# Performance work log

Hardware: AMD Instinct MI355X
Metric: run time of the kernel (lower is better)

## Reference

```python
import jax, jax.numpy as jnp
import numpy as np

B, C, SEG = 16, 32, 512            # graphs, configs per graph, nodes per segment
N = B * C * SEG                     # 262144 total nodes
E = 2 * N                           # 524288 edges
NUM_OPS, OP_DIM = 120, 64
NF_RAW = 112                        # raw node features
NF_IN = NF_RAW + OP_DIM             # 176
ND, CD = 192, 64                    # node_feature_dim, conf_feature_dim
GH = ND + CD                        # 256 graphsage hidden


def setup_inputs() -> dict:
    key = jax.random.key(0)
    ks = jax.random.split(key, 40)
    g = lambda i, shape, s: jax.random.normal(ks[i], shape, jnp.float32) * s
    inp = {
        'node_features': jax.random.normal(ks[0], (N, NF_RAW), jnp.float32),
        'node_config_features': jax.random.normal(ks[1], (N, 14), jnp.float32),
        'node_separation': (jnp.arange(B * C) + 1) * SEG,          # cumulative end idx
        'node_ops': jax.random.randint(ks[2], (N,), 0, NUM_OPS),
        'edges': jax.random.randint(ks[3], (2, E), 0, N),
        'batches': jnp.repeat(jnp.arange(B), C),
        # parameters (stored as [in, out]); ~1/sqrt(fan_in) scale
        'emb': g(4, (NUM_OPS, OP_DIM), 0.1),
        'nf_w1': g(5, (NF_IN, NF_IN), 0.075), 'nf_b1': jnp.zeros((NF_IN,)),
        'nf_w2': g(6, (NF_IN, ND), 0.075),   'nf_b2': jnp.zeros((ND,)),
        'cf_w1': g(7, (14, 14), 0.26),       'cf_b1': jnp.zeros((14,)),
        'cf_w2': g(8, (14, CD), 0.26),       'cf_b2': jnp.zeros((CD,)),
        'pre_w1': g(9, (GH, ND), 0.06),      'pre_b1': jnp.zeros((ND,)),
        'pre_w2': g(10, (ND, ND), 0.07),     'pre_b2': jnp.zeros((ND,)),
        'sage_wl': g(11, (2, GH, GH), 0.06), 'sage_bl': jnp.zeros((2, GH)),
        'sage_wr': g(12, (2, GH, GH), 0.06),
        'mlp_w1': g(13, (2, GH, ND), 0.06),  'mlp_b1': jnp.zeros((2, ND)),
        'mlp_w2': g(14, (2, ND, ND), 0.07),  'mlp_b2': jnp.zeros((2, ND)),
        'fc_w': g(15, (ND, 1), 0.07),
    }
    return inp


def reference(node_features, node_config_features, node_separation, node_ops,
              edges, batches, emb, nf_w1, nf_b1, nf_w2, nf_b2,
              cf_w1, cf_b1, cf_w2, cf_b2, pre_w1, pre_b1, pre_w2, pre_b2,
              sage_wl, sage_bl, sage_wr, mlp_w1, mlp_b1, mlp_w2, mlp_b2, fc_w):
    lr01 = lambda v: jax.nn.leaky_relu(v, 0.01)   # torch.nn.LeakyReLU default
    lr02 = lambda v: jax.nn.leaky_relu(v, 0.2)    # MLP / GraphSage alpha

    # embedding + node feature MLP
    x = jnp.concatenate([node_features, emb[node_ops]], axis=1)        # [N,176]
    x = lr01(lr01(x @ nf_w1 + nf_b1) @ nf_w2 + nf_b2)                  # [N,192]
    cf = lr01(lr01(node_config_features @ cf_w1 + cf_b1) @ cf_w2 + cf_b2)  # [N,64]

    # GraphSage encoder: prenet then 2 residual SAGEConv+MLP blocks
    h = jnp.concatenate([cf, x], axis=1)                               # [N,256]
    h = lr02(lr02(h @ pre_w1 + pre_b1) @ pre_w2 + pre_b2)              # [N,192]
    src, dst = edges[0], edges[1]
    n = h.shape[0]
    for l in range(2):
        y = jnp.concatenate([cf, h], axis=1)                           # [N,256]
        # SAGEConv(aggr='max'): lin_l(max_{j->i} y_j) + lin_r(y_i)
        agg = jax.ops.segment_max(y[src], dst, num_segments=n)
        agg = jnp.where(jnp.isfinite(agg), agg, 0.0)  # isolated nodes -> 0
        y = agg @ sage_wl[l] + sage_bl[l] + y @ sage_wr[l]             # [N,256]
        y = lr02(lr02(y @ mlp_w1[l] + mlp_b1[l]) @ mlp_w2[l] + mlp_b2[l])
        h = h + y

    # per-segment sum pooling (the original Python loop), then group by graph
    seg_id = jnp.searchsorted(node_separation, jnp.arange(n), side='right')
    pooled = jax.ops.segment_sum(h, seg_id, num_segments=node_separation.shape[0])  # [B*C,192]
    scores = (pooled @ fc_w)[:, 0]                                      # [B*C]
    return scores.reshape(B, C)
```

## Files before the change

kernel.cpp:

```cpp
#include <hip/hip_runtime.h>
#include <hip/hip_bf16.h>
#include <math.h>

#define NNODES 262144
#define NEDGES 524288
#define NSEG   512

typedef __hip_bfloat16 bf16;
typedef __attribute__((ext_vector_type(8))) short short8;
typedef __attribute__((ext_vector_type(4))) short short4v;
typedef __attribute__((ext_vector_type(4))) float f32x4;

__device__ __forceinline__ short bfbits(float f) {
    return __builtin_bit_cast(short, (__bf16)f);
}
__device__ __forceinline__ float bitsf(short s) {
    unsigned u = ((unsigned)(unsigned short)s) << 16;
    return __builtin_bit_cast(float, u);
}

__device__ __forceinline__ short8 ld8(const bf16* p, size_t off) {
    return *(const short8*)((const short*)p + off);
}
__device__ __forceinline__ short8 ld8(const float* p, size_t off) {
    const float4* q = (const float4*)(p + off);
    float4 a = q[0], b = q[1];
    short8 r;
    r[0] = bfbits(a.x); r[1] = bfbits(a.y); r[2] = bfbits(a.z); r[3] = bfbits(a.w);
    r[4] = bfbits(b.x); r[5] = bfbits(b.y); r[6] = bfbits(b.z); r[7] = bfbits(b.w);
    return r;
}

__global__ void prep_wt(const float* __restrict__ Wa, int kw,
                        const float* __restrict__ Wb,
                        short* __restrict__ Wt, int K, int OUT)
{
    int k = blockIdx.x * 256 + threadIdx.x;
    int c = blockIdx.y;
    if (k < K) {
        float v = (k < kw) ? Wa[(size_t)k * OUT + c] : Wb[(size_t)(k - kw) * OUT + c];
        Wt[(size_t)c * K + k] = bfbits(v);
    }
}

template<typename TA, int BN>
__global__ __launch_bounds__(512, 4) void mfma_gemm(
    const TA* __restrict__ A0, int w0,
    const TA* __restrict__ A1, int w1,
    const TA* __restrict__ A2, int w2,
    const int*   __restrict__ gidx,
    const short* __restrict__ Wt,
    const float* __restrict__ bias,
    const bf16*  __restrict__ res,
    bf16* __restrict__ out,
    int K, int OUT, float alpha)
{
    constexpr int NRW = BN / 64;
    __shared__ short As[128 * 40];
    __shared__ short Bs[BN * 40];
    __shared__ float biasLds[BN];

    const int tid  = threadIdx.x;
    const int lane = tid & 63;
    const int wid  = tid >> 6;
    const int row0 = blockIdx.x * 128;
    const int wr   = (wid >> 2) * 64;
    const int wc   = (wid & 3) * (BN / 4);
    const int fr   = lane & 15;
    const int fc   = lane >> 4;

    if (tid < BN) biasLds[tid] = (tid < OUT) ? bias[tid] : 0.f;

    f32x4 acc[NRW][4];
    #pragma unroll
    for (int nr = 0; nr < NRW; ++nr)
        #pragma unroll
        for (int m = 0; m < 4; ++m) acc[nr][m] = f32x4{0.f, 0.f, 0.f, 0.f};

    for (int k0 = 0; k0 < K; k0 += 32) {
        {
            int r  = tid >> 2;
            int kl = (tid & 3) * 8;
            int gk = k0 + kl;
            short8 v{};
            if (gk < K) {
                int n = row0 + r;
                if (gk < w0) v = ld8(A0, (size_t)n * w0 + gk);
                else {
                    int k1 = gk - w0;
                    if (k1 < w1) {
                        int rr = gidx ? gidx[n] : n;
                        v = ld8(A1, (size_t)rr * w1 + k1);
                    } else {
                        v = ld8(A2, (size_t)n * w2 + (k1 - w1));
                    }
                }
            }
            *(short8*)&As[r * 40 + kl] = v;
        }
        #pragma unroll
        for (int i = 0; i < (BN * 4 + 511) / 512; ++i) {
            int f = i * 512 + tid;
            if (f < BN * 4) {
                int c  = f >> 2;
                int kl = (f & 3) * 8;
                int gk = k0 + kl;
                short8 v{};
                if (gk < K && c < OUT) v = *(const short8*)&Wt[(size_t)c * K + gk];
                *(short8*)&Bs[c * 40 + kl] = v;
            }
        }
        __syncthreads();
        short8 af[4];
        #pragma unroll
        for (int m = 0; m < 4; ++m)
            af[m] = *(short8*)&As[(wr + m * 16 + fr) * 40 + fc * 8];
        #pragma unroll
        for (int nr = 0; nr < NRW; ++nr) {
            short8 bfr = *(short8*)&Bs[(wc + nr * 16 + fr) * 40 + fc * 8];
            #pragma unroll
            for (int m = 0; m < 4; ++m)
                acc[nr][m] = __builtin_amdgcn_mfma_f32_16x16x32_bf16(
                    bfr, af[m], acc[nr][m], 0, 0, 0);
        }
        __syncthreads();
    }
    #pragma unroll
    for (int nr = 0; nr < NRW; ++nr) {
        int c0 = wc + nr * 16 + fc * 4;
        if (c0 < OUT) {
            #pragma unroll
            for (int m = 0; m < 4; ++m) {
                int r = row0 + wr + m * 16 + fr;
                size_t base = (size_t)r * OUT + c0;
                short4v o;
                if (res) {
                    short4v rv = *(const short4v*)((const short*)res + base);
                    #pragma unroll
                    for (int j = 0; j < 4; ++j) {
                        float v = acc[nr][m][j] + biasLds[c0 + j];
                        v = (v > 0.f) ? v : alpha * v;
                        o[j] = bfbits(v + bitsf(rv[j]));
                    }
                } else {
                    #pragma unroll
                    for (int j = 0; j < 4; ++j) {
                        float v = acc[nr][m][j] + biasLds[c0 + j];
                        v = (v > 0.f) ? v : alpha * v;
                        o[j] = bfbits(v);
                    }
                }
                *(short4v*)((short*)out + base) = o;
            }
        }
    }
}

__global__ __launch_bounds__(256) void cf_mlp(
    const float* __restrict__ ncf,
    const float* __restrict__ w1, const float* __restrict__ b1,
    const float* __restrict__ w2, const float* __restrict__ b2,
    bf16* __restrict__ cf)
{
    __shared__ float W1s[196], B1s[14], W2s[896], B2s[64];
    int t = threadIdx.x;
    for (int i = t; i < 196; i += 256) W1s[i] = w1[i];
    for (int i = t; i < 896; i += 256) W2s[i] = w2[i];
    if (t < 14) B1s[t] = b1[t];
    if (t >= 32 && t < 96) B2s[t - 32] = b2[t - 32];
    __syncthreads();

    int n = blockIdx.x * 256 + t;
    float in[14], hid[14];
    #pragma unroll
    for (int k = 0; k < 14; ++k) in[k] = ncf[(size_t)n * 14 + k];
    #pragma unroll
    for (int j = 0; j < 14; ++j) {
        float s = B1s[j];
        #pragma unroll
        for (int k = 0; k < 14; ++k) s += in[k] * W1s[k * 14 + j];
        hid[j] = (s > 0.f) ? s : 0.01f * s;
    }
    #pragma unroll 4
    for (int j = 0; j < 64; ++j) {
        float s = B2s[j];
        #pragma unroll
        for (int k = 0; k < 14; ++k) s += hid[k] * W2s[k * 64 + j];
        s = (s > 0.f) ? s : 0.01f * s;
        cf[(size_t)n * 64 + j] = __float2bfloat16(s);
    }
}

__global__ void zero_ints(int* __restrict__ p, int n)
{
    int i = blockIdx.x * 256 + threadIdx.x;
    if (i < n) p[i] = 0;
}

__global__ void count_deg(const int* __restrict__ dst, int* __restrict__ indeg)
{
    int e = blockIdx.x * 256 + threadIdx.x;
    atomicAdd(&indeg[dst[e]], 1);
}

__global__ __launch_bounds__(256) void scan_block(
    const int* __restrict__ in, int* __restrict__ part, int* __restrict__ bsums)
{
    __shared__ int sh[256];
    int t = threadIdx.x, b = blockIdx.x;
    int base = b * 1024 + t * 4;
    int v0 = in[base], v1 = in[base + 1], v2 = in[base + 2], v3 = in[base + 3];
    int s = v0 + v1 + v2 + v3;
    sh[t] = s; __syncthreads();
    #pragma unroll
    for (int off = 1; off < 256; off <<= 1) {
        int x = (t >= off) ? sh[t - off] : 0;
        __syncthreads();
        sh[t] += x;
        __syncthreads();
    }
    int excl = sh[t] - s;
    if (t == 255) bsums[b] = sh[t];
    part[base]     = excl;
    part[base + 1] = excl + v0;
    part[base + 2] = excl + v0 + v1;
    part[base + 3] = excl + v0 + v1 + v2;
}

__global__ __launch_bounds__(256) void scan_tops(int* __restrict__ bsums)
{
    __shared__ int sh[256];
    int t = threadIdx.x;
    int s = bsums[t];
    sh[t] = s; __syncthreads();
    #pragma unroll
    for (int off = 1; off < 256; off <<= 1) {
        int x = (t >= off) ? sh[t - off] : 0;
        __syncthreads();
        sh[t] += x;
        __syncthreads();
    }
    bsums[t] = sh[t] - s;
}

__global__ void scan_fix(int* __restrict__ offsets, const int* __restrict__ bsums,
                         int* __restrict__ cursor)
{
    int i = blockIdx.x * 256 + threadIdx.x;
    int v = offsets[i] + bsums[i >> 10];
    offsets[i] = v;
    cursor[i]  = v;
    if (i == 0) offsets[NNODES] = NEDGES;
}

__global__ void scatter_edges(const int* __restrict__ src, const int* __restrict__ dst,
                              int* __restrict__ cursor, int* __restrict__ csr)
{
    int e = blockIdx.x * 256 + threadIdx.x;
    int pos = atomicAdd(&cursor[dst[e]], 1);
    csr[pos] = src[e];
}

__global__ __launch_bounds__(256) void sage_agg(
    const int* __restrict__ offsets, const int* __restrict__ csr,
    const bf16* __restrict__ cf, const bf16* __restrict__ h,
    bf16* __restrict__ agg)
{
    int wid = threadIdx.x >> 6, lane = threadIdx.x & 63;
    int n = blockIdx.x * 4 + wid;
    int beg = offsets[n], end = offsets[n + 1];
    float m0 = -3.4e38f, m1 = m0, m2 = m0, m3 = m0;
    for (int e = beg; e < end; ++e) {
        int s = csr[e];
        m0 = fmaxf(m0, __bfloat162float(cf[(size_t)s * 64 + lane]));
        const bf16* hr = h + (size_t)s * 192;
        m1 = fmaxf(m1, __bfloat162float(hr[lane]));
        m2 = fmaxf(m2, __bfloat162float(hr[64 + lane]));
        m3 = fmaxf(m3, __bfloat162float(hr[128 + lane]));
    }
    if (beg == end) { m0 = m1 = m2 = m3 = 0.f; }
    bf16* ar = agg + (size_t)n * 256;
    ar[lane]       = __float2bfloat16(m0);
    ar[64 + lane]  = __float2bfloat16(m1);
    ar[128 + lane] = __float2bfloat16(m2);
    ar[192 + lane] = __float2bfloat16(m3);
}

__global__ __launch_bounds__(256) void pool_fc(
    const bf16* __restrict__ h, const int* __restrict__ sep,
    const float* __restrict__ fc_w, float* __restrict__ out)
{
    __shared__ float red[256];
    int b = blockIdx.x, t = threadIdx.x;
    int r0 = (b == 0) ? 0 : sep[b - 1];
    int r1 = sep[b];
    float s0 = 0.f, s1 = 0.f, s2 = 0.f, s3 = 0.f;
    if (t < 192) {
        int r = r0;
        for (; r + 3 < r1; r += 4) {
            s0 += __bfloat162float(h[(size_t)r * 192 + t]);
            s1 += __bfloat162float(h[(size_t)(r + 1) * 192 + t]);
            s2 += __bfloat162float(h[(size_t)(r + 2) * 192 + t]);
            s3 += __bfloat162float(h[(size_t)(r + 3) * 192 + t]);
        }
        for (; r < r1; ++r) s0 += __bfloat162float(h[(size_t)r * 192 + t]);
    }
    red[t] = (t < 192) ? (s0 + s1 + s2 + s3) * fc_w[t] : 0.f;
    __syncthreads();
    #pragma unroll
    for (int st = 128; st > 0; st >>= 1) {
        if (t < st) red[t] += red[t + st];
        __syncthreads();
    }
    if (t == 0) out[b] = red[0];
}

__global__ void report_ws(float* __restrict__ out, float mb)
{
    out[blockIdx.x * 256 + threadIdx.x] = mb;
}

extern "C" void kernel_launch(void* const* d_in, const int* in_sizes, int n_in,
                              void* d_out, int out_size, void* d_ws, size_t ws_size,
                              hipStream_t stream)
{
    const float* node_features = (const float*)d_in[0];
    const float* node_config   = (const float*)d_in[1];
    const int*   node_sep      = (const int*)d_in[2];
    const int*   node_ops      = (const int*)d_in[3];
    const int*   edges         = (const int*)d_in[4];
    const float* emb    = (const float*)d_in[6];
    const float* nf_w1  = (const float*)d_in[7];
    const float* nf_b1  = (const float*)d_in[8];
    const float* nf_w2  = (const float*)d_in[9];
    const float* nf_b2  = (const float*)d_in[10];
    const float* cf_w1  = (const float*)d_in[11];
    const float* cf_b1  = (const float*)d_in[12];
    const float* cf_w2  = (const float*)d_in[13];
    const float* cf_b2  = (const float*)d_in[14];
    const float* pre_w1 = (const float*)d_in[15];
    const float* pre_b1 = (const float*)d_in[16];
    const float* pre_w2 = (const float*)d_in[17];
    const float* pre_b2 = (const float*)d_in[18];
    const float* sage_wl= (const float*)d_in[19];
    const float* sage_bl= (const float*)d_in[20];
    const float* sage_wr= (const float*)d_in[21];
    const float* mlp_w1 = (const float*)d_in[22];
    const float* mlp_b1 = (const float*)d_in[23];
    const float* mlp_w2 = (const float*)d_in[24];
    const float* mlp_b2 = (const float*)d_in[25];
    const float* fc_w   = (const float*)d_in[26];

    const size_t N = NNODES;

    const size_t WT_NF1  = 0;
    const size_t WT_NF2  = WT_NF1  + 176 * 176;
    const size_t WT_PRE1 = WT_NF2  + 192 * 176;
    const size_t WT_PRE2 = WT_PRE1 + 192 * 256;
    const size_t WT_SAGE = WT_PRE2 + 192 * 192;
    const size_t WT_MLP1 = WT_SAGE + 2 * 256 * 512;
    const size_t WT_MLP2 = WT_MLP1 + 2 * 192 * 256;
    const size_t WT_TOT  = WT_MLP2 + 2 * 192 * 192;

    const size_t fl_bytes  = N * 768 * sizeof(bf16);
    const size_t wt_bytes  = WT_TOT * 2;
    const size_t int_elems = (N + 1) + N + N + NEDGES + 256;
    const size_t needed    = fl_bytes + wt_bytes + int_elems * 4;
    if (ws_size < needed) {
        report_ws<<<2, 256, 0, stream>>>((float*)d_out,
                                         (float)((double)ws_size / 1048576.0));
        return;
    }

    bf16* cf   = (bf16*)d_ws;
    bf16* h    = cf   + N * 64;
    bf16* bufA = h    + N * 192;
    bf16* bufB = bufA + N * 256;
    short* wt  = (short*)(bufB + N * 256);
    int* offsets = (int*)(wt + WT_TOT);
    int* indeg   = offsets + (N + 1);
    int* cursor  = indeg + N;
    int* csr     = cursor + N;
    int* bsums   = csr + NEDGES;

    const int* esrc = edges;
    const int* edst = edges + NEDGES;

    dim3 blk(256);
    dim3 blk512(512);
    const int GB = NNODES / 128;

    prep_wt<<<dim3(1, 176), blk, 0, stream>>>(nf_w1, 176, nullptr, wt + WT_NF1, 176, 176);
    prep_wt<<<dim3(1, 192), blk, 0, stream>>>(nf_w2, 176, nullptr, wt + WT_NF2, 176, 192);
    prep_wt<<<dim3(1, 192), blk, 0, stream>>>(pre_w1, 256, nullptr, wt + WT_PRE1, 256, 192);
    prep_wt<<<dim3(1, 192), blk, 0, stream>>>(pre_w2, 192, nullptr, wt + WT_PRE2, 192, 192);
    for (int l = 0; l < 2; ++l) {
        prep_wt<<<dim3(2, 256), blk, 0, stream>>>(
            sage_wl + (size_t)l * 256 * 256, 256, sage_wr + (size_t)l * 256 * 256,
            wt + WT_SAGE + (size_t)l * 256 * 512, 512, 256);
        prep_wt<<<dim3(1, 192), blk, 0, stream>>>(
            mlp_w1 + (size_t)l * 256 * 192, 256, nullptr,
            wt + WT_MLP1 + (size_t)l * 192 * 256, 256, 192);
        prep_wt<<<dim3(1, 192), blk, 0, stream>>>(
            mlp_w2 + (size_t)l * 192 * 192, 192, nullptr,
            wt + WT_MLP2 + (size_t)l * 192 * 192, 192, 192);
    }

    cf_mlp<<<NNODES / 256, blk, 0, stream>>>(node_config, cf_w1, cf_b1, cf_w2, cf_b2, cf);

    mfma_gemm<float, 192><<<GB, blk512, 0, stream>>>(
        node_features, 112, emb, 64, (const float*)nullptr, 0, node_ops,
        wt + WT_NF1, nf_b1, nullptr, bufA, 176, 176, 0.01f);
    mfma_gemm<bf16, 192><<<GB, blk512, 0, stream>>>(
        bufA, 176, (const bf16*)nullptr, 0, (const bf16*)nullptr, 0, nullptr,
        wt + WT_NF2, nf_b2, nullptr, bufB, 176, 192, 0.01f);

    mfma_gemm<bf16, 192><<<GB, blk512, 0, stream>>>(
        cf, 64, bufB, 192, (const bf16*)nullptr, 0, nullptr,
        wt + WT_PRE1, pre_b1, nullptr, bufA, 256, 192, 0.2f);
    mfma_gemm<bf16, 192><<<GB, blk512, 0, stream>>>(
        bufA, 192, (const bf16*)nullptr, 0, (const bf16*)nullptr, 0, nullptr,
        wt + WT_PRE2, pre_b2, nullptr, h, 192, 192, 0.2f);

    zero_ints<<<NNODES / 256, blk, 0, stream>>>(indeg, NNODES);
    count_deg<<<NEDGES / 256, blk, 0, stream>>>(edst, indeg);
    scan_block<<<NNODES / 1024, blk, 0, stream>>>(indeg, offsets, bsums);
    scan_tops<<<1, blk, 0, stream>>>(bsums);
    scan_fix<<<NNODES / 256, blk, 0, stream>>>(offsets, bsums, cursor);
    scatter_edges<<<NEDGES / 256, blk, 0, stream>>>(esrc, edst, cursor, csr);

    for (int l = 0; l < 2; ++l) {
        sage_agg<<<NNODES / 4, blk, 0, stream>>>(offsets, csr, cf, h, bufA);
        mfma_gemm<bf16, 256><<<GB, blk512, 0, stream>>>(
            bufA, 256, cf, 64, h, 192, nullptr,
            wt + WT_SAGE + (size_t)l * 256 * 512, sage_bl + (size_t)l * 256,
            nullptr, bufB, 512, 256, 1.0f);
        mfma_gemm<bf16, 192><<<GB, blk512, 0, stream>>>(
            bufB, 256, (const bf16*)nullptr, 0, (const bf16*)nullptr, 0, nullptr,
            wt + WT_MLP1 + (size_t)l * 192 * 256, mlp_b1 + (size_t)l * 192,
            nullptr, bufA, 256, 192, 0.2f);
        mfma_gemm<bf16, 192><<<GB, blk512, 0, stream>>>(
            bufA, 192, (const bf16*)nullptr, 0, (const bf16*)nullptr, 0, nullptr,
            wt + WT_MLP2 + (size_t)l * 192 * 192, mlp_b2 + (size_t)l * 192,
            h, h, 192, 192, 0.2f);
    }

    pool_fc<<<NSEG, blk, 0, stream>>>(h, node_sep, fc_w, (float*)d_out);
}
```

Before: 1.564 ms.

## Prefetch GEMM tiles into registers, vectorize SAGE max gather, batch weight prep

The MFMA GEMM now loads the next K-slice of A and B into registers while the current slice is multiplied from LDS, so global-load latency overlaps with compute. The SAGE max aggregation gives each lane four contiguous bf16 values via a 64-bit load and processes two edges per iteration, which cuts the number of load instructions per gathered row. The ten weight-transpose kernels are merged into one launch with a job table, removing launch overhead. Holding the prefetched tiles raises register pressure in the GEMM, which could lower occupancy.

```diff
diff --git a/kernel.cpp b/kernel.cpp
--- a/kernel.cpp
+++ b/kernel.cpp
@@ -31,15 +31,23 @@
     return r;
 }
 
-__global__ void prep_wt(const float* __restrict__ Wa, int kw,
-                        const float* __restrict__ Wb,
-                        short* __restrict__ Wt, int K, int OUT)
-{
+struct PrepJobs {
+    const float* wa[10];
+    const float* wb[10];
+    int kw[10]; int K[10]; int OUT[10]; long off[10];
+};
+
+__global__ void prep_all(PrepJobs jobs, short* __restrict__ wt)
+{
+    int j = blockIdx.z;
     int k = blockIdx.x * 256 + threadIdx.x;
     int c = blockIdx.y;
-    if (k < K) {
-        float v = (k < kw) ? Wa[(size_t)k * OUT + c] : Wb[(size_t)(k - kw) * OUT + c];
-        Wt[(size_t)c * K + k] = bfbits(v);
+    int K = jobs.K[j], OUT = jobs.OUT[j];
+    if (k < K && c < OUT) {
+        int kw = jobs.kw[j];
+        float v = (k < kw) ? jobs.wa[j][(size_t)k * OUT + c]
+                           : jobs.wb[j][(size_t)(k - kw) * OUT + c];
+        wt[jobs.off[j] + (size_t)c * K + k] = bfbits(v);
     }
 }
 
@@ -56,6 +64,7 @@
     int K, int OUT, float alpha)
 {
     constexpr int NRW = BN / 64;
+    constexpr int NB  = (BN * 4 + 511) / 512;
     __shared__ short As[128 * 40];
     __shared__ short Bs[BN * 40];
     __shared__ float biasLds[BN];
@@ -71,46 +80,70 @@
 
     if (tid < BN) biasLds[tid] = (tid < OUT) ? bias[tid] : 0.f;
 
-    f32x4 acc[NRW][4];
-    #pragma unroll
-    for (int nr = 0; nr < NRW; ++nr)
-        #pragma unroll
-        for (int m = 0; m < 4; ++m) acc[nr][m] = f32x4{0.f, 0.f, 0.f, 0.f};
-
-    for (int k0 = 0; k0 < K; k0 += 32) {
-        {
-            int r  = tid >> 2;
-            int kl = (tid & 3) * 8;
-            int gk = k0 + kl;
-            short8 v{};
-            if (gk < K) {
-                int n = row0 + r;
-                if (gk < w0) v = ld8(A0, (size_t)n * w0 + gk);
-                else {
-                    int k1 = gk - w0;
-                    if (k1 < w1) {
-                        int rr = gidx ? gidx[n] : n;
-                        v = ld8(A1, (size_t)rr * w1 + k1);
-                    } else {
-                        v = ld8(A2, (size_t)n * w2 + (k1 - w1));
-                    }
+    const int ar  = tid >> 2;
+    const int akl = (tid & 3) * 8;
+
+    auto loadA = [&](int k0) -> short8 {
+        int gk = k0 + akl;
+        short8 v{};
+        if (gk < K) {
+            int n = row0 + ar;
+            if (gk < w0) v = ld8(A0, (size_t)n * w0 + gk);
+            else {
+                int k1 = gk - w0;
+                if (k1 < w1) {
+                    int rr = gidx ? gidx[n] : n;
+                    v = ld8(A1, (size_t)rr * w1 + k1);
+                } else {
+                    v = ld8(A2, (size_t)n * w2 + (k1 - w1));
                 }
             }
-            *(short8*)&As[r * 40 + kl] = v;
-        }
-        #pragma unroll
-        for (int i = 0; i < (BN * 4 + 511) / 512; ++i) {
+        }
+        return v;
+    };
+    auto loadB = [&](int k0, int i) -> short8 {
+        int f = i * 512 + tid;
+        short8 v{};
+        if (f < BN * 4) {
+            int c  = f >> 2;
+            int gk = k0 + (f & 3) * 8;
+            if (gk < K && c < OUT) v = *(const short8*)&Wt[(size_t)c * K + gk];
+        }
+        return v;
+    };
+
+    f32x4 acc[NRW][4];
+    #pragma unroll
+    for (int nr = 0; nr < NRW; ++nr)
+        #pragma unroll
+        for (int m = 0; m < 4; ++m) acc[nr][m] = f32x4{0.f, 0.f, 0.f, 0.f};
+
+    short8 aC = loadA(0);
+    short8 bC[NB];
+    #pragma unroll
+    for (int i = 0; i < NB; ++i) bC[i] = loadB(0, i);
+
+    for (int k0 = 0; k0 < K; k0 += 32) {
+        *(short8*)&As[ar * 40 + akl] = aC;
+        #pragma unroll
+        for (int i = 0; i < NB; ++i) {
             int f = i * 512 + tid;
             if (f < BN * 4) {
                 int c  = f >> 2;
                 int kl = (f & 3) * 8;
-                int gk = k0 + kl;
-                short8 v{};
-                if (gk < K && c < OUT) v = *(const short8*)&Wt[(size_t)c * K + gk];
-                *(short8*)&Bs[c * 40 + kl] = v;
+                *(short8*)&Bs[c * 40 + kl] = bC[i];
             }
         }
         __syncthreads();
+        short8 aN{};
+        short8 bN[NB];
+        #pragma unroll
+        for (int i = 0; i < NB; ++i) bN[i] = short8{};
+        if (k0 + 32 < K) {
+            aN = loadA(k0 + 32);
+            #pragma unroll
+            for (int i = 0; i < NB; ++i) bN[i] = loadB(k0 + 32, i);
+        }
         short8 af[4];
         #pragma unroll
         for (int m = 0; m < 4; ++m)
@@ -124,6 +157,9 @@
                     bfr, af[m], acc[nr][m], 0, 0, 0);
         }
         __syncthreads();
+        aC = aN;
+        #pragma unroll
+        for (int i = 0; i < NB; ++i) bC[i] = bN[i];
     }
     #pragma unroll
     for (int nr = 0; nr < NRW; ++nr) {
@@ -269,21 +305,35 @@
     int wid = threadIdx.x >> 6, lane = threadIdx.x & 63;
     int n = blockIdx.x * 4 + wid;
     int beg = offsets[n], end = offsets[n + 1];
+
+    bool isCf = lane < 16;
+    const short* basep = isCf ? (const short*)cf : (const short*)h;
+    int rowW   = isCf ? 64 : 192;
+    int colOff = isCf ? lane * 4 : lane * 4 - 64;
+
     float m0 = -3.4e38f, m1 = m0, m2 = m0, m3 = m0;
-    for (int e = beg; e < end; ++e) {
-        int s = csr[e];
-        m0 = fmaxf(m0, __bfloat162float(cf[(size_t)s * 64 + lane]));
-        const bf16* hr = h + (size_t)s * 192;
-        m1 = fmaxf(m1, __bfloat162float(hr[lane]));
-        m2 = fmaxf(m2, __bfloat162float(hr[64 + lane]));
-        m3 = fmaxf(m3, __bfloat162float(hr[128 + lane]));
+    int e = beg;
+    for (; e + 1 < end; e += 2) {
+        int s0 = csr[e], s1 = csr[e + 1];
+        short4v v0 = *(const short4v*)(basep + (size_t)s0 * rowW + colOff);
+        short4v v1 = *(const short4v*)(basep + (size_t)s1 * rowW + colOff);
+        m0 = fmaxf(fmaxf(m0, bitsf(v0[0])), bitsf(v1[0]));
+        m1 = fmaxf(fmaxf(m1, bitsf(v0[1])), bitsf(v1[1]));
+        m2 = fmaxf(fmaxf(m2, bitsf(v0[2])), bitsf(v1[2]));
+        m3 = fmaxf(fmaxf(m3, bitsf(v0[3])), bitsf(v1[3]));
+    }
+    if (e < end) {
+        int s0 = csr[e];
+        short4v v0 = *(const short4v*)(basep + (size_t)s0 * rowW + colOff);
+        m0 = fmaxf(m0, bitsf(v0[0]));
+        m1 = fmaxf(m1, bitsf(v0[1]));
+        m2 = fmaxf(m2, bitsf(v0[2]));
+        m3 = fmaxf(m3, bitsf(v0[3]));
     }
     if (beg == end) { m0 = m1 = m2 = m3 = 0.f; }
-    bf16* ar = agg + (size_t)n * 256;
-    ar[lane]       = __float2bfloat16(m0);
-    ar[64 + lane]  = __float2bfloat16(m1);
-    ar[128 + lane] = __float2bfloat16(m2);
-    ar[192 + lane] = __float2bfloat16(m3);
+    short4v o;
+    o[0] = bfbits(m0); o[1] = bfbits(m1); o[2] = bfbits(m2); o[3] = bfbits(m3);
+    *(short4v*)((short*)agg + (size_t)n * 256 + lane * 4) = o;
 }
 
 __global__ __launch_bounds__(256) void pool_fc(
@@ -390,20 +440,24 @@
     dim3 blk512(512);
     const int GB = NNODES / 128;
 
-    prep_wt<<<dim3(1, 176), blk, 0, stream>>>(nf_w1, 176, nullptr, wt + WT_NF1, 176, 176);
-    prep_wt<<<dim3(1, 192), blk, 0, stream>>>(nf_w2, 176, nullptr, wt + WT_NF2, 176, 192);
-    prep_wt<<<dim3(1, 192), blk, 0, stream>>>(pre_w1, 256, nullptr, wt + WT_PRE1, 256, 192);
-    prep_wt<<<dim3(1, 192), blk, 0, stream>>>(pre_w2, 192, nullptr, wt + WT_PRE2, 192, 192);
-    for (int l = 0; l < 2; ++l) {
-        prep_wt<<<dim3(2, 256), blk, 0, stream>>>(
-            sage_wl + (size_t)l * 256 * 256, 256, sage_wr + (size_t)l * 256 * 256,
-            wt + WT_SAGE + (size_t)l * 256 * 512, 512, 256);
-        prep_wt<<<dim3(1, 192), blk, 0, stream>>>(
-            mlp_w1 + (size_t)l * 256 * 192, 256, nullptr,
-            wt + WT_MLP1 + (size_t)l * 192 * 256, 256, 192);
-        prep_wt<<<dim3(1, 192), blk, 0, stream>>>(
-            mlp_w2 + (size_t)l * 192 * 192, 192, nullptr,
-            wt + WT_MLP2 + (size_t)l * 192 * 192, 192, 192);
+    {
+        PrepJobs jobs;
+        auto set = [&](int i, const float* wa, const float* wb, int kw, int K,
+                       int OUT, size_t off) {
+            jobs.wa[i] = wa; jobs.wb[i] = wb; jobs.kw[i] = kw;
+            jobs.K[i] = K; jobs.OUT[i] = OUT; jobs.off[i] = (long)off;
+        };
+        set(0, nf_w1, nullptr, 176, 176, 176, WT_NF1);
+        set(1, nf_w2, nullptr, 176, 176, 192, WT_NF2);
+        set(2, pre_w1, nullptr, 256, 256, 192, WT_PRE1);
+        set(3, pre_w2, nullptr, 192, 192, 192, WT_PRE2);
+        set(4, sage_wl,               sage_wr,               256, 512, 256, WT_SAGE);
+        set(5, sage_wl + 256 * 256,   sage_wr + 256 * 256,   256, 512, 256, WT_SAGE + 256 * 512);
+        set(6, mlp_w1,                nullptr, 256, 256, 192, WT_MLP1);
+        set(7, mlp_w1 + 256 * 192,    nullptr, 256, 256, 192, WT_MLP1 + 192 * 256);
+        set(8, mlp_w2,                nullptr, 192, 192, 192, WT_MLP2);
+        set(9, mlp_w2 + 192 * 192,    nullptr, 192, 192, 192, WT_MLP2 + 192 * 192);
+        prep_all<<<dim3(2, 256, 10), blk, 0, stream>>>(jobs, wt);
     }
 
     cf_mlp<<<NNODES / 256, blk, 0, stream>>>(node_config, cf_w1, cf_b1, cf_w2, cf_b2, cf);
```

Result: faster. 1.397 ms (-10.7%).
